# Optimization experiments

Measured on AMD Instinct MI355X. Metric: run time of the kernel, lower is better.

## Reference

```python
import jax, jax.numpy as jnp
import numpy as np

N_NODES = 50000
N_EDGES = 800000
IN_DIM = 128
HID = 128
N_GRAPHS = 64


def setup_inputs() -> dict:
    key = jax.random.key(0)
    ks = jax.random.split(key, 12)
    edge_index = jax.random.randint(ks[0], (2, N_EDGES), 0, N_NODES, dtype=jnp.int64)
    edge_weight = jax.random.uniform(ks[1], (N_EDGES,), dtype=jnp.float32)
    input_feature = jax.random.normal(ks[2], (N_NODES, IN_DIM), dtype=jnp.float32)
    graph_indicator = jnp.sort(jax.random.randint(ks[3], (N_NODES,), 0, N_GRAPHS, dtype=jnp.int64))
    s = 0.05
    W1 = jax.random.normal(ks[4], (IN_DIM, HID), dtype=jnp.float32) * s
    b1 = jnp.zeros((HID,), jnp.float32)
    W2 = jax.random.normal(ks[5], (HID, HID), dtype=jnp.float32) * s
    b2 = jnp.zeros((HID,), jnp.float32)
    W3 = jax.random.normal(ks[6], (HID, HID), dtype=jnp.float32) * s
    b3 = jnp.zeros((HID,), jnp.float32)
    wa = jax.random.normal(ks[7], (3 * HID, 1), dtype=jnp.float32) * s
    ba = jnp.zeros((1,), jnp.float32)
    Wf = jax.random.normal(ks[8], (3 * HID * 2, IN_DIM), dtype=jnp.float32) * s
    bf = jnp.zeros((IN_DIM,), jnp.float32)
    return dict(edge_index=edge_index, edge_weight=edge_weight,
                input_feature=input_feature, graph_indicator=graph_indicator,
                W1=W1, b1=b1, W2=W2, b2=b2, W3=W3, b3=b3,
                wa=wa, ba=ba, Wf=Wf, bf=bf)


def reference(edge_index, edge_weight, input_feature, graph_indicator,
              W1, b1, W2, b2, W3, b3, wa, ba, Wf, bf):
    src, dst = edge_index[0], edge_index[1]

    def gcn(x, W, b):
        # GraphConvolution: adj @ (x @ W) + b, adj given as weighted edge list
        support = x @ W  # [N, d_out]
        msg = edge_weight[:, None] * support[src]  # [E, d_out] gather
        return jax.ops.segment_sum(msg, dst, num_segments=N_NODES) + b

    g1 = jax.nn.relu(gcn(input_feature, W1, b1))
    g2 = jax.nn.relu(gcn(g1, W2, b2))
    g3 = jax.nn.relu(gcn(g2, W3, b3))
    h = jnp.concatenate([g1, g2, g3], axis=1)  # [N, 3*HID]

    # SelfAttentionPooling: attention score via a 1-dim GraphConvolution, tanh gate
    score = jnp.tanh(gcn(h, wa, ba))  # [N, 1]
    pool = h * score

    # segment avg / max pooling per graph
    seg_sum = jax.ops.segment_sum(pool, graph_indicator, num_segments=N_GRAPHS)
    counts = jax.ops.segment_sum(jnp.ones((N_NODES, 1), pool.dtype), graph_indicator,
                                 num_segments=N_GRAPHS)
    avg = seg_sum / jnp.maximum(counts, 1.0)
    mx = jax.ops.segment_max(pool, graph_indicator, num_segments=N_GRAPHS)
    pooled = jnp.concatenate([avg, mx], axis=1)  # [G, 6*HID]

    return jax.nn.relu(pooled @ Wf + bf)  # [G, IN_DIM]
```

## Files before the change

kernel.cpp:

```cpp
#include <hip/hip_runtime.h>
#include <math.h>

#define HID 128
#define POOL_SEG 16
#define WT_STRIDE 136
#define ELL_D 48
#define SC_CHUNK 2048
#define FXS 16384.0f
#define FXI (1.0f/16384.0f)

typedef __attribute__((ext_vector_type(8))) short short8;
typedef __attribute__((ext_vector_type(4))) float float4v;

__device__ inline short f2bf(float f) {
  unsigned u = __builtin_bit_cast(unsigned, f);
  unsigned r = (u + 0x7fff + ((u >> 16) & 1)) >> 16;
  return (short)r;
}
__device__ inline unsigned pack2bf(float lo, float hi) {
  return (unsigned)(unsigned short)f2bf(lo) | ((unsigned)(unsigned short)f2bf(hi) << 16);
}
__device__ inline float bflo(unsigned u) { return __builtin_bit_cast(float, u << 16); }
__device__ inline float bfhi(unsigned u) { return __builtin_bit_cast(float, u & 0xffff0000u); }
__device__ inline float bf2f(unsigned short s) { return __builtin_bit_cast(float, (unsigned)s << 16); }
__device__ inline unsigned short f2h(float f) {
  _Float16 h = (_Float16)f;
  return __builtin_bit_cast(unsigned short, h);
}
__device__ inline float h2f(unsigned short hb) {
  return (float)__builtin_bit_cast(_Float16, hb);
}

__global__ __launch_bounds__(256) void prologue(
    const void* __restrict__ ei_raw, const float* __restrict__ ew,
    int2* __restrict__ packed,
    const float* __restrict__ W1, const float* __restrict__ W2, const float* __restrict__ W3,
    short* __restrict__ T1, short* __restrict__ T2, short* __restrict__ T3,
    const void* __restrict__ gi_raw, int* __restrict__ gstart,
    int E, int N, int G, int EB) {
  int b = blockIdx.x, t = threadIdx.x;
  if (b < EB) {
    int e = b * 256 + t;
    if (e < E) {
      const int* pw = (const int*)ei_raw;
      int nz = 0;
#pragma unroll
      for (int i = 1; i < 64; i += 2) nz |= pw[i];
      int s, d;
      if (nz == 0) {
        const long long* p = (const long long*)ei_raw;
        s = (int)p[e]; d = (int)p[E + e];
      } else {
        const int* p = (const int*)ei_raw;
        s = p[e]; d = p[E + e];
      }
      packed[e] = make_int2((d << 16) | s, __builtin_bit_cast(int, ew[e]));
    }
  } else if (b < EB + 192) {
    int i = (b - EB) * 256 + t;
    int which = i >> 14, idx = i & 16383;
    int k = idx >> 7, nn = idx & 127;
    const float* W = (which == 0) ? W1 : ((which == 1) ? W2 : W3);
    short* T = (which == 0) ? T1 : ((which == 1) ? T2 : T3);
    T[nn * WT_STRIDE + k] = f2bf(W[idx]);
  } else {
    int g = t;
    if (g > G) return;
    if (g == G) { gstart[g] = N; return; }
    bool is64 = (((const int*)gi_raw)[N - 1] == 0);
    const long long* g64 = (const long long*)gi_raw;
    const int* g32 = (const int*)gi_raw;
    int lo = 0, hi = N;
    while (lo < hi) {
      int mid = (lo + hi) >> 1;
      long long v = is64 ? g64[mid] : (long long)g32[mid];
      if (v < (long long)g) lo = mid + 1; else hi = mid;
    }
    gstart[g] = lo;
  }
}

__global__ void scatter_ell(const int2* __restrict__ packed, int* __restrict__ cursor,
                            unsigned* __restrict__ ell, int E, int N) {
  int group = blockIdx.x & 7;
  int chunk = blockIdx.x >> 3;
  int rng = (N + 7) >> 3;
  int lo = group * rng;
  int hi = lo + rng; if (hi > N) hi = N;
  int base = chunk * SC_CHUNK;
  for (int i = 0; i < SC_CHUNK; i += 256) {
    int e = base + i + threadIdx.x;
    if (e < E) {
      int2 rec = packed[e];
      int d = ((unsigned)rec.x) >> 16;
      if (d >= lo && d < hi) {
        unsigned s = (unsigned)rec.x & 0xFFFFu;
        unsigned short wh = f2h(__builtin_bit_cast(float, rec.y));
        int pos = atomicAdd(&cursor[d], 1);
        if (pos < ELL_D)
          ell[(size_t)d * ELL_D + pos] = (s << 16) | (unsigned)wh;
      }
    }
  }
}

__global__ __launch_bounds__(256) void gemm_mfma(const float* __restrict__ Af,
                                                 const unsigned short* __restrict__ Abf,
                                                 const short* __restrict__ Wt,
                                                 unsigned short* __restrict__ C,
                                                 int n, int a_is_bf16) {
  __shared__ short Wlds[128 * WT_STRIDE];
  int t = threadIdx.x;
  {
    const ulonglong2* gsrc = (const ulonglong2*)Wt;
    ulonglong2* ldst = (ulonglong2*)Wlds;
    for (int i = t; i < (128 * WT_STRIDE) / 8; i += 256) ldst[i] = gsrc[i];
  }
  __syncthreads();

  int wave = t >> 6, lane = t & 63;
  int quad = lane >> 4, l15 = lane & 15;
  int m0 = blockIdx.x * 64 + wave * 16;
  size_t SL = (size_t)n * 32;

  int m = m0 + l15; if (m >= n) m = n - 1;
  short8 afrag[4];
  if (a_is_bf16) {
#pragma unroll
    for (int c = 0; c < 4; c++)
      afrag[c] = *(const short8*)(Abf + c * SL + (size_t)m * 32 + quad * 8);
  } else {
    const float* Arow = Af + (size_t)m * 128;
#pragma unroll
    for (int c = 0; c < 4; c++) {
      int k0 = c * 32 + quad * 8;
      float4 x = *(const float4*)(Arow + k0);
      float4 y = *(const float4*)(Arow + k0 + 4);
      short8 a;
      a[0] = f2bf(x.x); a[1] = f2bf(x.y); a[2] = f2bf(x.z); a[3] = f2bf(x.w);
      a[4] = f2bf(y.x); a[5] = f2bf(y.y); a[6] = f2bf(y.z); a[7] = f2bf(y.w);
      afrag[c] = a;
    }
  }

  float4v acc[8];
#pragma unroll
  for (int tt = 0; tt < 8; tt++) acc[tt] = (float4v){0.f, 0.f, 0.f, 0.f};

#pragma unroll
  for (int c = 0; c < 4; c++) {
    int kb = c * 32 + quad * 8;
#pragma unroll
    for (int tt = 0; tt < 8; tt++) {
      const short8* bp = (const short8*)&Wlds[(tt * 16 + l15) * WT_STRIDE + kb];
      acc[tt] = __builtin_amdgcn_mfma_f32_16x16x32_bf16(afrag[c], *bp, acc[tt], 0, 0, 0);
    }
  }

  int rbase = m0 + quad * 4;
#pragma unroll
  for (int tt = 0; tt < 8; tt++) {
    int within = (tt & 1) * 16 + l15;
    size_t sb = (size_t)(tt >> 1) * SL;
#pragma unroll
    for (int r = 0; r < 4; r++) {
      int row = rbase + r;
      if (row < n) C[sb + (size_t)row * 32 + within] = (unsigned short)f2bf(acc[tt][r]);
    }
  }
}

#define ACC8(wv, vv)                                                          \
  acc[0] += rintf(wv * bflo(vv.x)); acc[1] += rintf(wv * bfhi(vv.x));        \
  acc[2] += rintf(wv * bflo(vv.y)); acc[3] += rintf(wv * bfhi(vv.y));        \
  acc[4] += rintf(wv * bflo(vv.z)); acc[5] += rintf(wv * bfhi(vv.z));        \
  acc[6] += rintf(wv * bflo(vv.w)); acc[7] += rintf(wv * bfhi(vv.w));

__global__ __launch_bounds__(256) void aggregate_sl(
    const unsigned short* __restrict__ support, const int* __restrict__ deg_arr,
    const unsigned* __restrict__ ell, const float* __restrict__ bias,
    unsigned short* __restrict__ out,
    const unsigned short* __restrict__ g1p, const unsigned short* __restrict__ g2p,
    const float* __restrict__ wa, int* __restrict__ s_pre_fx,
    int n, int halfN, int do_score) {
  int group = blockIdx.x & 7;
  int slice = group >> 1, half = group & 1;
  int chunk = blockIdx.x >> 3;
  int t = threadIdx.x;
  int local = chunk * 64 + (t >> 2);
  int q = t & 3;
  if (local >= halfN) return;
  int node = half * halfN + local;
  if (node >= n) return;

  int deg = deg_arr[node]; if (deg > ELL_D) deg = ELL_D;
  const unsigned* row = ell + (size_t)node * ELL_D;
  const uint4* sb = (const uint4*)support + (size_t)slice * n * 4 + q;

  float acc[8];
#pragma unroll
  for (int j = 0; j < 8; j++) acc[j] = 0.f;

  int i = 0;
  for (; i + 7 < deg; i += 8) {
    uint4 ra = *(const uint4*)(row + i);
    uint4 rb = *(const uint4*)(row + i + 4);
    uint4 v0 = sb[(size_t)(ra.x >> 16) * 4];
    uint4 v1 = sb[(size_t)(ra.y >> 16) * 4];
    uint4 v2 = sb[(size_t)(ra.z >> 16) * 4];
    uint4 v3 = sb[(size_t)(ra.w >> 16) * 4];
    uint4 v4 = sb[(size_t)(rb.x >> 16) * 4];
    uint4 v5 = sb[(size_t)(rb.y >> 16) * 4];
    uint4 v6 = sb[(size_t)(rb.z >> 16) * 4];
    uint4 v7 = sb[(size_t)(rb.w >> 16) * 4];
    float w0 = h2f((unsigned short)(ra.x & 0xFFFF)) * FXS;
    float w1 = h2f((unsigned short)(ra.y & 0xFFFF)) * FXS;
    float w2 = h2f((unsigned short)(ra.z & 0xFFFF)) * FXS;
    float w3 = h2f((unsigned short)(ra.w & 0xFFFF)) * FXS;
    float w4 = h2f((unsigned short)(rb.x & 0xFFFF)) * FXS;
    float w5 = h2f((unsigned short)(rb.y & 0xFFFF)) * FXS;
    float w6 = h2f((unsigned short)(rb.z & 0xFFFF)) * FXS;
    float w7 = h2f((unsigned short)(rb.w & 0xFFFF)) * FXS;
    ACC8(w0, v0) ACC8(w1, v1) ACC8(w2, v2) ACC8(w3, v3)
    ACC8(w4, v4) ACC8(w5, v5) ACC8(w6, v6) ACC8(w7, v7)
  }
  for (; i + 3 < deg; i += 4) {
    uint4 ra = *(const uint4*)(row + i);
    uint4 v0 = sb[(size_t)(ra.x >> 16) * 4];
    uint4 v1 = sb[(size_t)(ra.y >> 16) * 4];
    uint4 v2 = sb[(size_t)(ra.z >> 16) * 4];
    uint4 v3 = sb[(size_t)(ra.w >> 16) * 4];
    float w0 = h2f((unsigned short)(ra.x & 0xFFFF)) * FXS;
    float w1 = h2f((unsigned short)(ra.y & 0xFFFF)) * FXS;
    float w2 = h2f((unsigned short)(ra.z & 0xFFFF)) * FXS;
    float w3 = h2f((unsigned short)(ra.w & 0xFFFF)) * FXS;
    ACC8(w0, v0) ACC8(w1, v1) ACC8(w2, v2) ACC8(w3, v3)
  }
  for (; i < deg; i++) {
    unsigned r0 = row[i];
    float w0 = h2f((unsigned short)(r0 & 0xFFFF)) * FXS;
    uint4 v0 = sb[(size_t)(r0 >> 16) * 4];
    ACC8(w0, v0)
  }

  float f[8];
#pragma unroll
  for (int j = 0; j < 8; j++) f[j] = acc[j] * FXI;

  float4 b0 = ((const float4*)bias)[slice * 8 + q * 2];
  float4 b1 = ((const float4*)bias)[slice * 8 + q * 2 + 1];
  f[0] = fmaxf(f[0] + b0.x, 0.f); f[1] = fmaxf(f[1] + b0.y, 0.f);
  f[2] = fmaxf(f[2] + b0.z, 0.f); f[3] = fmaxf(f[3] + b0.w, 0.f);
  f[4] = fmaxf(f[4] + b1.x, 0.f); f[5] = fmaxf(f[5] + b1.y, 0.f);
  f[6] = fmaxf(f[6] + b1.z, 0.f); f[7] = fmaxf(f[7] + b1.w, 0.f);

  uint4 o;
  o.x = pack2bf(f[0], f[1]); o.y = pack2bf(f[2], f[3]);
  o.z = pack2bf(f[4], f[5]); o.w = pack2bf(f[6], f[7]);
  ((uint4*)out)[(size_t)slice * n * 4 + (size_t)node * 4 + q] = o;

  if (do_score) {
    uint4 u1 = ((const uint4*)g1p)[(size_t)slice * n * 4 + (size_t)node * 4 + q];
    uint4 u2 = ((const uint4*)g2p)[(size_t)slice * n * 4 + (size_t)node * 4 + q];
    const float* wa1 = wa + slice * 32 + q * 8;
    const float* wa2 = wa1 + 128;
    const float* wa3 = wa1 + 256;
    float sc = bflo(u1.x) * wa1[0] + bfhi(u1.x) * wa1[1]
             + bflo(u1.y) * wa1[2] + bfhi(u1.y) * wa1[3]
             + bflo(u1.z) * wa1[4] + bfhi(u1.z) * wa1[5]
             + bflo(u1.w) * wa1[6] + bfhi(u1.w) * wa1[7]
             + bflo(u2.x) * wa2[0] + bfhi(u2.x) * wa2[1]
             + bflo(u2.y) * wa2[2] + bfhi(u2.y) * wa2[3]
             + bflo(u2.z) * wa2[4] + bfhi(u2.z) * wa2[5]
             + bflo(u2.w) * wa2[6] + bfhi(u2.w) * wa2[7];
#pragma unroll
    for (int j = 0; j < 8; j++) sc += f[j] * wa3[j];
    sc += __shfl_xor(sc, 1, 64);
    sc += __shfl_xor(sc, 2, 64);
    if (q == 0) atomicAdd(&s_pre_fx[node], __float2int_rn(sc * FXS));
  }
}

__global__ __launch_bounds__(384) void pool_partial(const unsigned short* __restrict__ g1,
                                                    const unsigned short* __restrict__ g2,
                                                    const unsigned short* __restrict__ g3,
                                                    const int* __restrict__ s_pre_fx,
                                                    const int* __restrict__ deg_arr,
                                                    const unsigned* __restrict__ ell,
                                                    const float* __restrict__ ba,
                                                    const int* __restrict__ gstart,
                                                    float* __restrict__ part, int n) {
  int g = blockIdx.x / POOL_SEG, seg = blockIdx.x % POOL_SEG;
  int t = threadIdx.x;
  int sg = t >> 7, dd = t & 127;
  const unsigned short* gp = (sg == 0) ? g1 : ((sg == 1) ? g2 : g3);
  const unsigned short* col = gp + (size_t)(dd >> 5) * ((size_t)n * 32) + (dd & 31);
  int s = gstart[g], e = gstart[g + 1];
  int len = e - s;
  int chunk = (len + POOL_SEG - 1) / POOL_SEG;
  int ns = s + seg * chunk;
  int ne = ns + chunk; if (ne > e) ne = e;
  float ba0 = ba[0];
  __shared__ float sc_lds[256];
  float sum = 0.f, mx = -3.402823466e38f;
  for (int tb = ns; tb < ne; tb += 256) {
    int te = tb + 256; if (te > ne) te = ne;
    __syncthreads();
    if (t < te - tb) {
      int node = tb + t;
      int deg = deg_arr[node]; if (deg > ELL_D) deg = ELL_D;
      const unsigned* row = ell + (size_t)node * ELL_D;
      float acc = 0.f;
      for (int i = 0; i < deg; i++) {
        unsigned r = row[i];
        acc += rintf(h2f((unsigned short)(r & 0xFFFF)) * (float)s_pre_fx[r >> 16]);
      }
      sc_lds[t] = tanhf(acc * FXI + ba0);
    }
    __syncthreads();
    for (int node = tb; node < te; node++) {
      float v = bf2f(col[(size_t)node * 32]) * sc_lds[node - tb];
      sum += v;
      mx = fmaxf(mx, v);
    }
  }
  size_t base = (size_t)blockIdx.x * 768;
  part[base + t] = sum;
  part[base + 384 + t] = mx;
}

__global__ __launch_bounds__(512) void tail(const float* __restrict__ part,
                                            const int* __restrict__ gstart,
                                            const float* __restrict__ Wf,
                                            const float* __restrict__ bfb,
                                            float* __restrict__ out) {
  __shared__ float pooled[768];
  __shared__ float red[512];
  int g = blockIdx.x, t = threadIdx.x;
  float cnt = (float)(gstart[g + 1] - gstart[g]);
  float inv = 1.0f / fmaxf(cnt, 1.0f);
  if (t < 384) {
    int d = t;
    float sum = 0.f, mx = -3.402823466e38f;
    for (int seg = 0; seg < POOL_SEG; seg++) {
      size_t base = ((size_t)g * POOL_SEG + seg) * 768;
      sum += part[base + d];
      mx = fmaxf(mx, part[base + 384 + d]);
    }
    pooled[d] = sum * inv;
    pooled[384 + d] = mx;
  }
  __syncthreads();
  int kc = t >> 7, c = t & 127;
  float acc = (kc == 0) ? bfb[c] : 0.f;
  int k0 = kc * 192;
#pragma unroll 8
  for (int k = k0; k < k0 + 192; k++) acc += pooled[k] * Wf[(size_t)k * 128 + c];
  red[t] = acc;
  __syncthreads();
  if (t < 128)
    out[(size_t)g * 128 + t] =
        fmaxf(red[t] + red[t + 128] + red[t + 256] + red[t + 384], 0.f);
}

extern "C" void kernel_launch(void* const* d_in, const int* in_sizes, int n_in,
                              void* d_out, int out_size, void* d_ws, size_t ws_size,
                              hipStream_t stream) {
  const void* ei_raw = d_in[0];
  const float* ew    = (const float*)d_in[1];
  const float* X     = (const float*)d_in[2];
  const void* gi_raw = d_in[3];
  const float* W1 = (const float*)d_in[4];  const float* b1 = (const float*)d_in[5];
  const float* W2 = (const float*)d_in[6];  const float* b2 = (const float*)d_in[7];
  const float* W3 = (const float*)d_in[8];  const float* b3 = (const float*)d_in[9];
  const float* wa = (const float*)d_in[10]; const float* ba = (const float*)d_in[11];
  const float* Wf = (const float*)d_in[12]; const float* bf = (const float*)d_in[13];
  float* out = (float*)d_out;

  const int E = in_sizes[1];
  const int N = in_sizes[2] / 128;
  const int G = out_size / 128;

  char* ws = (char*)d_ws;
  size_t off = 0;
  auto take = [&](size_t bytes) {
    char* p = ws + off;
    off = (off + bytes + 255) & ~(size_t)255;
    return p;
  };
  int* zb = (int*)take((size_t)N * 8);
  int* cursor   = zb;
  int* s_pre_fx = zb + N;
  int2* packed  = (int2*)take((size_t)E * 8);
  unsigned* ell = (unsigned*)take((size_t)N * ELL_D * 4);
  short*    wt1 = (short*)take((size_t)128 * WT_STRIDE * 2);
  short*    wt2 = (short*)take((size_t)128 * WT_STRIDE * 2);
  short*    wt3 = (short*)take((size_t)128 * WT_STRIDE * 2);
  unsigned short* support = (unsigned short*)take((size_t)N * 128 * 2);
  unsigned short* g1      = (unsigned short*)take((size_t)N * 128 * 2);
  unsigned short* g2      = (unsigned short*)take((size_t)N * 128 * 2);
  unsigned short* g3      = (unsigned short*)take((size_t)N * 128 * 2);
  int*   gstart  = (int*)take((size_t)(G + 1) * 4);
  float* part    = (float*)take((size_t)G * POOL_SEG * 768 * 4);
  if (off > ws_size) return;

  hipMemsetAsync(zb, 0, (size_t)N * 8, stream);

  const int EB = (E + 255) / 256;
  prologue<<<EB + 192 + 1, 256, 0, stream>>>(ei_raw, ew, packed,
                                             W1, W2, W3, wt1, wt2, wt3,
                                             gi_raw, gstart, E, N, G, EB);
  {
    int chunks = (E + SC_CHUNK - 1) / SC_CHUNK;
    scatter_ell<<<8 * chunks, 256, 0, stream>>>(packed, cursor, ell, E, N);
  }

  const int GB = (N + 63) / 64;
  const int halfN = (N + 1) / 2;
  const int AGB = 8 * ((halfN + 63) / 64);
  gemm_mfma<<<GB, 256, 0, stream>>>(X, (const unsigned short*)nullptr, wt1, support, N, 0);
  aggregate_sl<<<AGB, 256, 0, stream>>>(support, cursor, ell, b1, g1,
                                        nullptr, nullptr, nullptr, nullptr, N, halfN, 0);
  gemm_mfma<<<GB, 256, 0, stream>>>((const float*)nullptr, g1, wt2, support, N, 1);
  aggregate_sl<<<AGB, 256, 0, stream>>>(support, cursor, ell, b2, g2,
                                        nullptr, nullptr, nullptr, nullptr, N, halfN, 0);
  gemm_mfma<<<GB, 256, 0, stream>>>((const float*)nullptr, g2, wt3, support, N, 1);
  aggregate_sl<<<AGB, 256, 0, stream>>>(support, cursor, ell, b3, g3,
                                        g1, g2, wa, s_pre_fx, N, halfN, 1);

  pool_partial<<<G * POOL_SEG, 384, 0, stream>>>(g1, g2, g3, s_pre_fx, cursor, ell,
                                                 ba, gstart, part, N);
  tail<<<G, 512, 0, stream>>>(part, gstart, Wf, bf, out);
}
```

Measured before the change: 318.6 us.

## Fuse memset into prologue, scatter into first GEMM, and tail into pool

```diff
diff --git a/kernel.cpp b/kernel.cpp
--- a/kernel.cpp
+++ b/kernel.cpp
@@ -33,15 +33,17 @@
 
 __global__ __launch_bounds__(256) void prologue(
     const void* __restrict__ ei_raw, const float* __restrict__ ew,
-    int2* __restrict__ packed,
+    int2* __restrict__ packed, int* __restrict__ cursor, int* __restrict__ s_pre_fx,
+    int* __restrict__ pool_done,
     const float* __restrict__ W1, const float* __restrict__ W2, const float* __restrict__ W3,
     short* __restrict__ T1, short* __restrict__ T2, short* __restrict__ T3,
     const void* __restrict__ gi_raw, int* __restrict__ gstart,
     int E, int N, int G, int EB) {
   int b = blockIdx.x, t = threadIdx.x;
   if (b < EB) {
-    int e = b * 256 + t;
-    if (e < E) {
+    int gid = b * 256 + t;
+    if (gid < N) { cursor[gid] = 0; s_pre_fx[gid] = 0; }
+    if (gid < E) {
       const int* pw = (const int*)ei_raw;
       int nz = 0;
 #pragma unroll
@@ -49,12 +51,12 @@
       int s, d;
       if (nz == 0) {
         const long long* p = (const long long*)ei_raw;
-        s = (int)p[e]; d = (int)p[E + e];
+        s = (int)p[gid]; d = (int)p[E + gid];
       } else {
         const int* p = (const int*)ei_raw;
-        s = p[e]; d = p[E + e];
+        s = p[gid]; d = p[E + gid];
       }
-      packed[e] = make_int2((d << 16) | s, __builtin_bit_cast(int, ew[e]));
+      packed[gid] = make_int2((d << 16) | s, __builtin_bit_cast(int, ew[gid]));
     }
   } else if (b < EB + 192) {
     int i = (b - EB) * 256 + t;
@@ -65,6 +67,7 @@
     T[nn * WT_STRIDE + k] = f2bf(W[idx]);
   } else {
     int g = t;
+    if (g < G) pool_done[g] = 0;
     if (g > G) return;
     if (g == G) { gstart[g] = N; return; }
     bool is64 = (((const int*)gi_raw)[N - 1] == 0);
@@ -80,35 +83,38 @@
   }
 }
 
-__global__ void scatter_ell(const int2* __restrict__ packed, int* __restrict__ cursor,
-                            unsigned* __restrict__ ell, int E, int N) {
-  int group = blockIdx.x & 7;
-  int chunk = blockIdx.x >> 3;
-  int rng = (N + 7) >> 3;
-  int lo = group * rng;
-  int hi = lo + rng; if (hi > N) hi = N;
-  int base = chunk * SC_CHUNK;
-  for (int i = 0; i < SC_CHUNK; i += 256) {
-    int e = base + i + threadIdx.x;
-    if (e < E) {
-      int2 rec = packed[e];
-      int d = ((unsigned)rec.x) >> 16;
-      if (d >= lo && d < hi) {
-        unsigned s = (unsigned)rec.x & 0xFFFFu;
-        unsigned short wh = f2h(__builtin_bit_cast(float, rec.y));
-        int pos = atomicAdd(&cursor[d], 1);
-        if (pos < ELL_D)
-          ell[(size_t)d * ELL_D + pos] = (s << 16) | (unsigned)wh;
-      }
-    }
-  }
-}
-
 __global__ __launch_bounds__(256) void gemm_mfma(const float* __restrict__ Af,
                                                  const unsigned short* __restrict__ Abf,
                                                  const short* __restrict__ Wt,
                                                  unsigned short* __restrict__ C,
-                                                 int n, int a_is_bf16) {
+                                                 int n, int a_is_bf16, int gemm_nb,
+                                                 const int2* __restrict__ packed,
+                                                 int* __restrict__ cursor,
+                                                 unsigned* __restrict__ ell, int E) {
+  if (blockIdx.x >= gemm_nb) {
+    int sb = blockIdx.x - gemm_nb;
+    int group = sb & 7;
+    int chunk = sb >> 3;
+    int rng = (n + 7) >> 3;
+    int lo = group * rng;
+    int hi = lo + rng; if (hi > n) hi = n;
+    int base = chunk * SC_CHUNK;
+    for (int i = 0; i < SC_CHUNK; i += 256) {
+      int e = base + i + threadIdx.x;
+      if (e < E) {
+        int2 rec = packed[e];
+        int d = ((unsigned)rec.x) >> 16;
+        if (d >= lo && d < hi) {
+          unsigned s = (unsigned)rec.x & 0xFFFFu;
+          unsigned short wh = f2h(__builtin_bit_cast(float, rec.y));
+          int pos = atomicAdd(&cursor[d], 1);
+          if (pos < ELL_D)
+            ell[(size_t)d * ELL_D + pos] = (s << 16) | (unsigned)wh;
+        }
+      }
+    }
+    return;
+  }
   __shared__ short Wlds[128 * WT_STRIDE];
   int t = threadIdx.x;
   {
@@ -281,15 +287,19 @@
   }
 }
 
-__global__ __launch_bounds__(384) void pool_partial(const unsigned short* __restrict__ g1,
-                                                    const unsigned short* __restrict__ g2,
-                                                    const unsigned short* __restrict__ g3,
-                                                    const int* __restrict__ s_pre_fx,
-                                                    const int* __restrict__ deg_arr,
-                                                    const unsigned* __restrict__ ell,
-                                                    const float* __restrict__ ba,
-                                                    const int* __restrict__ gstart,
-                                                    float* __restrict__ part, int n) {
+__global__ __launch_bounds__(384) void pool_tail(const unsigned short* __restrict__ g1,
+                                                 const unsigned short* __restrict__ g2,
+                                                 const unsigned short* __restrict__ g3,
+                                                 const int* __restrict__ s_pre_fx,
+                                                 const int* __restrict__ deg_arr,
+                                                 const unsigned* __restrict__ ell,
+                                                 const float* __restrict__ ba,
+                                                 const int* __restrict__ gstart,
+                                                 float* __restrict__ part,
+                                                 int* __restrict__ pool_done,
+                                                 const float* __restrict__ Wf,
+                                                 const float* __restrict__ bfb,
+                                                 float* __restrict__ out, int n) {
   int g = blockIdx.x / POOL_SEG, seg = blockIdx.x % POOL_SEG;
   int t = threadIdx.x;
   int sg = t >> 7, dd = t & 127;
@@ -327,40 +337,40 @@
   size_t base = (size_t)blockIdx.x * 768;
   part[base + t] = sum;
   part[base + 384 + t] = mx;
-}
-
-__global__ __launch_bounds__(512) void tail(const float* __restrict__ part,
-                                            const int* __restrict__ gstart,
-                                            const float* __restrict__ Wf,
-                                            const float* __restrict__ bfb,
-                                            float* __restrict__ out) {
+
+  __threadfence();
+  __shared__ int is_last;
+  __syncthreads();
+  if (t == 0) is_last = (atomicAdd(&pool_done[g], 1) == POOL_SEG - 1) ? 1 : 0;
+  __syncthreads();
+  if (!is_last) return;
+  __threadfence();
+
   __shared__ float pooled[768];
-  __shared__ float red[512];
-  int g = blockIdx.x, t = threadIdx.x;
-  float cnt = (float)(gstart[g + 1] - gstart[g]);
+  __shared__ float red[384];
+  float cnt = (float)len;
   float inv = 1.0f / fmaxf(cnt, 1.0f);
-  if (t < 384) {
+  {
     int d = t;
-    float sum = 0.f, mx = -3.402823466e38f;
-    for (int seg = 0; seg < POOL_SEG; seg++) {
-      size_t base = ((size_t)g * POOL_SEG + seg) * 768;
-      sum += part[base + d];
-      mx = fmaxf(mx, part[base + 384 + d]);
-    }
-    pooled[d] = sum * inv;
-    pooled[384 + d] = mx;
+    float ssum = 0.f, smx = -3.402823466e38f;
+    for (int sg2 = 0; sg2 < POOL_SEG; sg2++) {
+      size_t b2 = ((size_t)g * POOL_SEG + sg2) * 768;
+      ssum += part[b2 + d];
+      smx = fmaxf(smx, part[b2 + 384 + d]);
+    }
+    pooled[d] = ssum * inv;
+    pooled[384 + d] = smx;
   }
   __syncthreads();
   int kc = t >> 7, c = t & 127;
   float acc = (kc == 0) ? bfb[c] : 0.f;
-  int k0 = kc * 192;
+  int k0 = kc * 256;
 #pragma unroll 8
-  for (int k = k0; k < k0 + 192; k++) acc += pooled[k] * Wf[(size_t)k * 128 + c];
+  for (int k = k0; k < k0 + 256; k++) acc += pooled[k] * Wf[(size_t)k * 128 + c];
   red[t] = acc;
   __syncthreads();
   if (t < 128)
-    out[(size_t)g * 128 + t] =
-        fmaxf(red[t] + red[t + 128] + red[t + 256] + red[t + 384], 0.f);
+    out[(size_t)g * 128 + t] = fmaxf(red[t] + red[t + 128] + red[t + 256], 0.f);
 }
 
 extern "C" void kernel_launch(void* const* d_in, const int* in_sizes, int n_in,
@@ -388,9 +398,8 @@
     off = (off + bytes + 255) & ~(size_t)255;
     return p;
   };
-  int* zb = (int*)take((size_t)N * 8);
-  int* cursor   = zb;
-  int* s_pre_fx = zb + N;
+  int* cursor   = (int*)take((size_t)N * 4);
+  int* s_pre_fx = (int*)take((size_t)N * 4);
   int2* packed  = (int2*)take((size_t)E * 8);
   unsigned* ell = (unsigned*)take((size_t)N * ELL_D * 4);
   short*    wt1 = (short*)take((size_t)128 * WT_STRIDE * 2);
@@ -400,35 +409,33 @@
   unsigned short* g1      = (unsigned short*)take((size_t)N * 128 * 2);
   unsigned short* g2      = (unsigned short*)take((size_t)N * 128 * 2);
   unsigned short* g3      = (unsigned short*)take((size_t)N * 128 * 2);
-  int*   gstart  = (int*)take((size_t)(G + 1) * 4);
-  float* part    = (float*)take((size_t)G * POOL_SEG * 768 * 4);
+  int*   gstart    = (int*)take((size_t)(G + 1) * 4);
+  int*   pool_done = (int*)take((size_t)G * 4);
+  float* part      = (float*)take((size_t)G * POOL_SEG * 768 * 4);
   if (off > ws_size) return;
 
-  hipMemsetAsync(zb, 0, (size_t)N * 8, stream);
-
   const int EB = (E + 255) / 256;
-  prologue<<<EB + 192 + 1, 256, 0, stream>>>(ei_raw, ew, packed,
-                                             W1, W2, W3, wt1, wt2, wt3,
+  prologue<<<EB + 192 + 1, 256, 0, stream>>>(ei_raw, ew, packed, cursor, s_pre_fx,
+                                             pool_done, W1, W2, W3, wt1, wt2, wt3,
                                              gi_raw, gstart, E, N, G, EB);
-  {
-    int chunks = (E + SC_CHUNK - 1) / SC_CHUNK;
-    scatter_ell<<<8 * chunks, 256, 0, stream>>>(packed, cursor, ell, E, N);
-  }
 
   const int GB = (N + 63) / 64;
   const int halfN = (N + 1) / 2;
   const int AGB = 8 * ((halfN + 63) / 64);
-  gemm_mfma<<<GB, 256, 0, stream>>>(X, (const unsigned short*)nullptr, wt1, support, N, 0);
+  const int chunks = (E + SC_CHUNK - 1) / SC_CHUNK;
+  gemm_mfma<<<GB + 8 * chunks, 256, 0, stream>>>(X, (const unsigned short*)nullptr, wt1,
+                                                 support, N, 0, GB, packed, cursor, ell, E);
   aggregate_sl<<<AGB, 256, 0, stream>>>(support, cursor, ell, b1, g1,
                                         nullptr, nullptr, nullptr, nullptr, N, halfN, 0);
-  gemm_mfma<<<GB, 256, 0, stream>>>((const float*)nullptr, g1, wt2, support, N, 1);
+  gemm_mfma<<<GB, 256, 0, stream>>>((const float*)nullptr, g1, wt2, support, N, 1, GB,
+                                    nullptr, nullptr, nullptr, 0);
   aggregate_sl<<<AGB, 256, 0, stream>>>(support, cursor, ell, b2, g2,
                                         nullptr, nullptr, nullptr, nullptr, N, halfN, 0);
-  gemm_mfma<<<GB, 256, 0, stream>>>((const float*)nullptr, g2, wt3, support, N, 1);
+  gemm_mfma<<<GB, 256, 0, stream>>>((const float*)nullptr, g2, wt3, support, N, 1, GB,
+                                    nullptr, nullptr, nullptr, 0);
   aggregate_sl<<<AGB, 256, 0, stream>>>(support, cursor, ell, b3, g3,
                                         g1, g2, wa, s_pre_fx, N, halfN, 1);
 
-  pool_partial<<<G * POOL_SEG, 384, 0, stream>>>(g1, g2, g3, s_pre_fx, cursor, ell,
-                                                 ba, gstart, part, N);
-  tail<<<G, 512, 0, stream>>>(part, gstart, Wf, bf, out);
-}
+  pool_tail<<<G * POOL_SEG, 384, 0, stream>>>(g1, g2, g3, s_pre_fx, cursor, ell,
+                                              ba, gstart, part, pool_done, Wf, bf, out, N);
+}
```

Measured after the change: 444.8 us. 1.4x slower.

## Fuse ELL scatter into first GEMM launch and zero buffers in prologue

Applied to the files above, without the earlier changes.

```diff
diff --git a/kernel.cpp b/kernel.cpp
--- a/kernel.cpp
+++ b/kernel.cpp
@@ -33,15 +33,16 @@
 
 __global__ __launch_bounds__(256) void prologue(
     const void* __restrict__ ei_raw, const float* __restrict__ ew,
-    int2* __restrict__ packed,
+    int2* __restrict__ packed, int* __restrict__ cursor, int* __restrict__ s_pre_fx,
     const float* __restrict__ W1, const float* __restrict__ W2, const float* __restrict__ W3,
     short* __restrict__ T1, short* __restrict__ T2, short* __restrict__ T3,
     const void* __restrict__ gi_raw, int* __restrict__ gstart,
     int E, int N, int G, int EB) {
   int b = blockIdx.x, t = threadIdx.x;
   if (b < EB) {
-    int e = b * 256 + t;
-    if (e < E) {
+    int gid = b * 256 + t;
+    if (gid < N) { cursor[gid] = 0; s_pre_fx[gid] = 0; }
+    if (gid < E) {
       const int* pw = (const int*)ei_raw;
       int nz = 0;
 #pragma unroll
@@ -49,12 +50,12 @@
       int s, d;
       if (nz == 0) {
         const long long* p = (const long long*)ei_raw;
-        s = (int)p[e]; d = (int)p[E + e];
+        s = (int)p[gid]; d = (int)p[E + gid];
       } else {
         const int* p = (const int*)ei_raw;
-        s = p[e]; d = p[E + e];
+        s = p[gid]; d = p[E + gid];
       }
-      packed[e] = make_int2((d << 16) | s, __builtin_bit_cast(int, ew[e]));
+      packed[gid] = make_int2((d << 16) | s, __builtin_bit_cast(int, ew[gid]));
     }
   } else if (b < EB + 192) {
     int i = (b - EB) * 256 + t;
@@ -80,35 +81,38 @@
   }
 }
 
-__global__ void scatter_ell(const int2* __restrict__ packed, int* __restrict__ cursor,
-                            unsigned* __restrict__ ell, int E, int N) {
-  int group = blockIdx.x & 7;
-  int chunk = blockIdx.x >> 3;
-  int rng = (N + 7) >> 3;
-  int lo = group * rng;
-  int hi = lo + rng; if (hi > N) hi = N;
-  int base = chunk * SC_CHUNK;
-  for (int i = 0; i < SC_CHUNK; i += 256) {
-    int e = base + i + threadIdx.x;
-    if (e < E) {
-      int2 rec = packed[e];
-      int d = ((unsigned)rec.x) >> 16;
-      if (d >= lo && d < hi) {
-        unsigned s = (unsigned)rec.x & 0xFFFFu;
-        unsigned short wh = f2h(__builtin_bit_cast(float, rec.y));
-        int pos = atomicAdd(&cursor[d], 1);
-        if (pos < ELL_D)
-          ell[(size_t)d * ELL_D + pos] = (s << 16) | (unsigned)wh;
-      }
-    }
-  }
-}
-
 __global__ __launch_bounds__(256) void gemm_mfma(const float* __restrict__ Af,
                                                  const unsigned short* __restrict__ Abf,
                                                  const short* __restrict__ Wt,
                                                  unsigned short* __restrict__ C,
-                                                 int n, int a_is_bf16) {
+                                                 int n, int a_is_bf16, int gemm_nb,
+                                                 const int2* __restrict__ packed,
+                                                 int* __restrict__ cursor,
+                                                 unsigned* __restrict__ ell, int E) {
+  if (blockIdx.x >= gemm_nb) {
+    int sb = blockIdx.x - gemm_nb;
+    int group = sb & 7;
+    int chunk = sb >> 3;
+    int rng = (n + 7) >> 3;
+    int lo = group * rng;
+    int hi = lo + rng; if (hi > n) hi = n;
+    int base = chunk * SC_CHUNK;
+    for (int i = 0; i < SC_CHUNK; i += 256) {
+      int e = base + i + threadIdx.x;
+      if (e < E) {
+        int2 rec = packed[e];
+        int d = ((unsigned)rec.x) >> 16;
+        if (d >= lo && d < hi) {
+          unsigned s = (unsigned)rec.x & 0xFFFFu;
+          unsigned short wh = f2h(__builtin_bit_cast(float, rec.y));
+          int pos = atomicAdd(&cursor[d], 1);
+          if (pos < ELL_D)
+            ell[(size_t)d * ELL_D + pos] = (s << 16) | (unsigned)wh;
+        }
+      }
+    }
+    return;
+  }
   __shared__ short Wlds[128 * WT_STRIDE];
   int t = threadIdx.x;
   {
@@ -388,9 +392,8 @@
     off = (off + bytes + 255) & ~(size_t)255;
     return p;
   };
-  int* zb = (int*)take((size_t)N * 8);
-  int* cursor   = zb;
-  int* s_pre_fx = zb + N;
+  int* cursor   = (int*)take((size_t)N * 4);
+  int* s_pre_fx = (int*)take((size_t)N * 4);
   int2* packed  = (int2*)take((size_t)E * 8);
   unsigned* ell = (unsigned*)take((size_t)N * ELL_D * 4);
   short*    wt1 = (short*)take((size_t)128 * WT_STRIDE * 2);
@@ -404,27 +407,25 @@
   float* part    = (float*)take((size_t)G * POOL_SEG * 768 * 4);
   if (off > ws_size) return;
 
-  hipMemsetAsync(zb, 0, (size_t)N * 8, stream);
-
   const int EB = (E + 255) / 256;
-  prologue<<<EB + 192 + 1, 256, 0, stream>>>(ei_raw, ew, packed,
+  prologue<<<EB + 192 + 1, 256, 0, stream>>>(ei_raw, ew, packed, cursor, s_pre_fx,
                                              W1, W2, W3, wt1, wt2, wt3,
                                              gi_raw, gstart, E, N, G, EB);
-  {
-    int chunks = (E + SC_CHUNK - 1) / SC_CHUNK;
-    scatter_ell<<<8 * chunks, 256, 0, stream>>>(packed, cursor, ell, E, N);
-  }
 
   const int GB = (N + 63) / 64;
   const int halfN = (N + 1) / 2;
   const int AGB = 8 * ((halfN + 63) / 64);
-  gemm_mfma<<<GB, 256, 0, stream>>>(X, (const unsigned short*)nullptr, wt1, support, N, 0);
+  const int chunks = (E + SC_CHUNK - 1) / SC_CHUNK;
+  gemm_mfma<<<GB + 8 * chunks, 256, 0, stream>>>(X, (const unsigned short*)nullptr, wt1,
+                                                 support, N, 0, GB, packed, cursor, ell, E);
   aggregate_sl<<<AGB, 256, 0, stream>>>(support, cursor, ell, b1, g1,
                                         nullptr, nullptr, nullptr, nullptr, N, halfN, 0);
-  gemm_mfma<<<GB, 256, 0, stream>>>((const float*)nullptr, g1, wt2, support, N, 1);
+  gemm_mfma<<<GB, 256, 0, stream>>>((const float*)nullptr, g1, wt2, support, N, 1, GB,
+                                    nullptr, nullptr, nullptr, 0);
   aggregate_sl<<<AGB, 256, 0, stream>>>(support, cursor, ell, b2, g2,
                                         nullptr, nullptr, nullptr, nullptr, N, halfN, 0);
-  gemm_mfma<<<GB, 256, 0, stream>>>((const float*)nullptr, g2, wt3, support, N, 1);
+  gemm_mfma<<<GB, 256, 0, stream>>>((const float*)nullptr, g2, wt3, support, N, 1, GB,
+                                    nullptr, nullptr, nullptr, 0);
   aggregate_sl<<<AGB, 256, 0, stream>>>(support, cursor, ell, b3, g3,
                                         g1, g2, wa, s_pre_fx, N, halfN, 1);
 
```

New measurement: 310.4 us. -2.6%, faster.

## Fuse prologue, ELL scatter and first GEMM into one launch; unroll aggregation by 16

Applied to the files above, without the earlier changes.

```diff
diff --git a/kernel.cpp b/kernel.cpp
--- a/kernel.cpp
+++ b/kernel.cpp
@@ -31,90 +31,77 @@
   return (float)__builtin_bit_cast(_Float16, hb);
 }
 
-__global__ __launch_bounds__(256) void prologue(
+__global__ __launch_bounds__(256) void mega1(
+    const float* __restrict__ Af, const short* __restrict__ WtUnused,
+    unsigned short* __restrict__ C, int n, int gemm_nb,
     const void* __restrict__ ei_raw, const float* __restrict__ ew,
-    int2* __restrict__ packed,
+    int* __restrict__ cursor, unsigned* __restrict__ ell, int E, int scb,
     const float* __restrict__ W1, const float* __restrict__ W2, const float* __restrict__ W3,
-    short* __restrict__ T1, short* __restrict__ T2, short* __restrict__ T3,
-    const void* __restrict__ gi_raw, int* __restrict__ gstart,
-    int E, int N, int G, int EB) {
-  int b = blockIdx.x, t = threadIdx.x;
-  if (b < EB) {
-    int e = b * 256 + t;
-    if (e < E) {
+    short* __restrict__ T2, short* __restrict__ T3,
+    const void* __restrict__ gi_raw, int* __restrict__ gstart, int G) {
+  int t = threadIdx.x;
+  if (blockIdx.x >= gemm_nb) {
+    int b2 = blockIdx.x - gemm_nb;
+    if (b2 < scb) {
+      int group = b2 & 7;
+      int chunk = b2 >> 3;
+      int rng = (n + 7) >> 3;
+      int lo = group * rng;
+      int hi = lo + rng; if (hi > n) hi = n;
       const int* pw = (const int*)ei_raw;
       int nz = 0;
 #pragma unroll
       for (int i = 1; i < 64; i += 2) nz |= pw[i];
-      int s, d;
-      if (nz == 0) {
-        const long long* p = (const long long*)ei_raw;
-        s = (int)p[e]; d = (int)p[E + e];
-      } else {
-        const int* p = (const int*)ei_raw;
-        s = p[e]; d = p[E + e];
+      bool is64 = (nz == 0);
+      const long long* p64 = (const long long*)ei_raw;
+      const int* p32 = (const int*)ei_raw;
+      int base = chunk * SC_CHUNK;
+      for (int i = 0; i < SC_CHUNK; i += 256) {
+        int e = base + i + t;
+        if (e < E) {
+          int s, d;
+          if (is64) { s = (int)p64[e]; d = (int)p64[E + e]; }
+          else      { s = p32[e];      d = p32[E + e]; }
+          if (d >= lo && d < hi) {
+            unsigned short wh = f2h(ew[e]);
+            int pos = atomicAdd(&cursor[d], 1);
+            if (pos < ELL_D)
+              ell[(size_t)d * ELL_D + pos] = ((unsigned)s << 16) | (unsigned)wh;
+          }
+        }
       }
-      packed[e] = make_int2((d << 16) | s, __builtin_bit_cast(int, ew[e]));
-    }
-  } else if (b < EB + 192) {
-    int i = (b - EB) * 256 + t;
-    int which = i >> 14, idx = i & 16383;
-    int k = idx >> 7, nn = idx & 127;
-    const float* W = (which == 0) ? W1 : ((which == 1) ? W2 : W3);
-    short* T = (which == 0) ? T1 : ((which == 1) ? T2 : T3);
-    T[nn * WT_STRIDE + k] = f2bf(W[idx]);
-  } else {
+      return;
+    }
+    b2 -= scb;
+    if (b2 < 128) {
+      int i = b2 * 256 + t;
+      int which = i >> 14, idx = i & 16383;
+      int k = idx >> 7, nn = idx & 127;
+      const float* W = (which == 0) ? W2 : W3;
+      short* T = (which == 0) ? T2 : T3;
+      T[nn * WT_STRIDE + k] = f2bf(W[idx]);
+      return;
+    }
     int g = t;
     if (g > G) return;
-    if (g == G) { gstart[g] = N; return; }
-    bool is64 = (((const int*)gi_raw)[N - 1] == 0);
+    if (g == G) { gstart[g] = n; return; }
+    bool gis64 = (((const int*)gi_raw)[n - 1] == 0);
     const long long* g64 = (const long long*)gi_raw;
     const int* g32 = (const int*)gi_raw;
-    int lo = 0, hi = N;
+    int lo = 0, hi = n;
     while (lo < hi) {
       int mid = (lo + hi) >> 1;
-      long long v = is64 ? g64[mid] : (long long)g32[mid];
+      long long v = gis64 ? g64[mid] : (long long)g32[mid];
       if (v < (long long)g) lo = mid + 1; else hi = mid;
     }
     gstart[g] = lo;
-  }
-}
-
-__global__ void scatter_ell(const int2* __restrict__ packed, int* __restrict__ cursor,
-                            unsigned* __restrict__ ell, int E, int N) {
-  int group = blockIdx.x & 7;
-  int chunk = blockIdx.x >> 3;
-  int rng = (N + 7) >> 3;
-  int lo = group * rng;
-  int hi = lo + rng; if (hi > N) hi = N;
-  int base = chunk * SC_CHUNK;
-  for (int i = 0; i < SC_CHUNK; i += 256) {
-    int e = base + i + threadIdx.x;
-    if (e < E) {
-      int2 rec = packed[e];
-      int d = ((unsigned)rec.x) >> 16;
-      if (d >= lo && d < hi) {
-        unsigned s = (unsigned)rec.x & 0xFFFFu;
-        unsigned short wh = f2h(__builtin_bit_cast(float, rec.y));
-        int pos = atomicAdd(&cursor[d], 1);
-        if (pos < ELL_D)
-          ell[(size_t)d * ELL_D + pos] = (s << 16) | (unsigned)wh;
-      }
-    }
-  }
-}
-
-__global__ __launch_bounds__(256) void gemm_mfma(const float* __restrict__ Af,
-                                                 const unsigned short* __restrict__ Abf,
-                                                 const short* __restrict__ Wt,
-                                                 unsigned short* __restrict__ C,
-                                                 int n, int a_is_bf16) {
+    return;
+  }
+
   __shared__ short Wlds[128 * WT_STRIDE];
-  int t = threadIdx.x;
-  {
-    const ulonglong2* gsrc = (const ulonglong2*)Wt;
-    ulonglong2* ldst = (ulonglong2*)Wlds;
-    for (int i = t; i < (128 * WT_STRIDE) / 8; i += 256) ldst[i] = gsrc[i];
+  for (int idx = t; idx < 16384; idx += 256) {
+    int k = idx >> 7, nn = idx & 127;
+    Wlds[nn * WT_STRIDE + k] = f2bf(W1[idx]);
   }
   __syncthreads();
 
@@ -125,11 +112,7 @@
 
   int m = m0 + l15; if (m >= n) m = n - 1;
   short8 afrag[4];
-  if (a_is_bf16) {
-#pragma unroll
-    for (int c = 0; c < 4; c++)
-      afrag[c] = *(const short8*)(Abf + c * SL + (size_t)m * 32 + quad * 8);
-  } else {
+  {
     const float* Arow = Af + (size_t)m * 128;
 #pragma unroll
     for (int c = 0; c < 4; c++) {
@@ -170,13 +153,63 @@
   }
 }
 
+__global__ __launch_bounds__(256) void gemm_mfma(const unsigned short* __restrict__ Abf,
+                                                 const short* __restrict__ Wt,
+                                                 unsigned short* __restrict__ C, int n) {
+  __shared__ short Wlds[128 * WT_STRIDE];
+  int t = threadIdx.x;
+  {
+    const ulonglong2* gsrc = (const ulonglong2*)Wt;
+    ulonglong2* ldst = (ulonglong2*)Wlds;
+    for (int i = t; i < (128 * WT_STRIDE) / 8; i += 256) ldst[i] = gsrc[i];
+  }
+  __syncthreads();
+
+  int wave = t >> 6, lane = t & 63;
+  int quad = lane >> 4, l15 = lane & 15;
+  int m0 = blockIdx.x * 64 + wave * 16;
+  size_t SL = (size_t)n * 32;
+
+  int m = m0 + l15; if (m >= n) m = n - 1;
+  short8 afrag[4];
+#pragma unroll
+  for (int c = 0; c < 4; c++)
+    afrag[c] = *(const short8*)(Abf + c * SL + (size_t)m * 32 + quad * 8);
+
+  float4v acc[8];
+#pragma unroll
+  for (int tt = 0; tt < 8; tt++) acc[tt] = (float4v){0.f, 0.f, 0.f, 0.f};
+
+#pragma unroll
+  for (int c = 0; c < 4; c++) {
+    int kb = c * 32 + quad * 8;
+#pragma unroll
+    for (int tt = 0; tt < 8; tt++) {
+      const short8* bp = (const short8*)&Wlds[(tt * 16 + l15) * WT_STRIDE + kb];
+      acc[tt] = __builtin_amdgcn_mfma_f32_16x16x32_bf16(afrag[c], *bp, acc[tt], 0, 0, 0);
+    }
+  }
+
+  int rbase = m0 + quad * 4;
+#pragma unroll
+  for (int tt = 0; tt < 8; tt++) {
+    int within = (tt & 1) * 16 + l15;
+    size_t sb = (size_t)(tt >> 1) * SL;
+#pragma unroll
+    for (int r = 0; r < 4; r++) {
+      int row = rbase + r;
+      if (row < n) C[sb + (size_t)row * 32 + within] = (unsigned short)f2bf(acc[tt][r]);
+    }
+  }
+}
+
 #define ACC8(wv, vv)                                                          \
   acc[0] += rintf(wv * bflo(vv.x)); acc[1] += rintf(wv * bfhi(vv.x));        \
   acc[2] += rintf(wv * bflo(vv.y)); acc[3] += rintf(wv * bfhi(vv.y));        \
   acc[4] += rintf(wv * bflo(vv.z)); acc[5] += rintf(wv * bfhi(vv.z));        \
   acc[6] += rintf(wv * bflo(vv.w)); acc[7] += rintf(wv * bfhi(vv.w));
 
-__global__ __launch_bounds__(256) void aggregate_sl(
+__global__ __launch_bounds__(256, 4) void aggregate_sl(
     const unsigned short* __restrict__ support, const int* __restrict__ deg_arr,
     const unsigned* __restrict__ ell, const float* __restrict__ bias,
     unsigned short* __restrict__ out,
@@ -202,6 +235,48 @@
   for (int j = 0; j < 8; j++) acc[j] = 0.f;
 
   int i = 0;
+  for (; i + 15 < deg; i += 16) {
+    uint4 ra = *(const uint4*)(row + i);
+    uint4 rb = *(const uint4*)(row + i + 4);
+    uint4 rc = *(const uint4*)(row + i + 8);
+    uint4 rd = *(const uint4*)(row + i + 12);
+    uint4 v0 = sb[(size_t)(ra.x >> 16) * 4];
+    uint4 v1 = sb[(size_t)(ra.y >> 16) * 4];
+    uint4 v2 = sb[(size_t)(ra.z >> 16) * 4];
+    uint4 v3 = sb[(size_t)(ra.w >> 16) * 4];
+    uint4 v4 = sb[(size_t)(rb.x >> 16) * 4];
+    uint4 v5 = sb[(size_t)(rb.y >> 16) * 4];
+    uint4 v6 = sb[(size_t)(rb.z >> 16) * 4];
+    uint4 v7 = sb[(size_t)(rb.w >> 16) * 4];
+    uint4 v8 = sb[(size_t)(rc.x >> 16) * 4];
+    uint4 v9 = sb[(size_t)(rc.y >> 16) * 4];
+    uint4 vA = sb[(size_t)(rc.z >> 16) * 4];
+    uint4 vB = sb[(size_t)(rc.w >> 16) * 4];
+    uint4 vC = sb[(size_t)(rd.x >> 16) * 4];
+    uint4 vD = sb[(size_t)(rd.y >> 16) * 4];
+    uint4 vE = sb[(size_t)(rd.z >> 16) * 4];
+    uint4 vF = sb[(size_t)(rd.w >> 16) * 4];
+    float w0 = h2f((unsigned short)(ra.x & 0xFFFF)) * FXS;
+    float w1 = h2f((unsigned short)(ra.y & 0xFFFF)) * FXS;
+    float w2 = h2f((unsigned short)(ra.z & 0xFFFF)) * FXS;
+    float w3 = h2f((unsigned short)(ra.w & 0xFFFF)) * FXS;
+    float w4 = h2f((unsigned short)(rb.x & 0xFFFF)) * FXS;
+    float w5 = h2f((unsigned short)(rb.y & 0xFFFF)) * FXS;
+    float w6 = h2f((unsigned short)(rb.z & 0xFFFF)) * FXS;
+    float w7 = h2f((unsigned short)(rb.w & 0xFFFF)) * FXS;
+    float w8 = h2f((unsigned short)(rc.x & 0xFFFF)) * FXS;
+    float w9 = h2f((unsigned short)(rc.y & 0xFFFF)) * FXS;
+    float wA = h2f((unsigned short)(rc.z & 0xFFFF)) * FXS;
+    float wB = h2f((unsigned short)(rc.w & 0xFFFF)) * FXS;
+    float wC = h2f((unsigned short)(rd.x & 0xFFFF)) * FXS;
+    float wD = h2f((unsigned short)(rd.y & 0xFFFF)) * FXS;
+    float wE = h2f((unsigned short)(rd.z & 0xFFFF)) * FXS;
+    float wF = h2f((unsigned short)(rd.w & 0xFFFF)) * FXS;
+    ACC8(w0, v0) ACC8(w1, v1) ACC8(w2, v2) ACC8(w3, v3)
+    ACC8(w4, v4) ACC8(w5, v5) ACC8(w6, v6) ACC8(w7, v7)
+    ACC8(w8, v8) ACC8(w9, v9) ACC8(wA, vA) ACC8(wB, vB)
+    ACC8(wC, vC) ACC8(wD, vD) ACC8(wE, vE) ACC8(wF, vF)
+  }
   for (; i + 7 < deg; i += 8) {
     uint4 ra = *(const uint4*)(row + i);
     uint4 rb = *(const uint4*)(row + i + 4);
@@ -391,9 +466,7 @@
   int* zb = (int*)take((size_t)N * 8);
   int* cursor   = zb;
   int* s_pre_fx = zb + N;
-  int2* packed  = (int2*)take((size_t)E * 8);
   unsigned* ell = (unsigned*)take((size_t)N * ELL_D * 4);
-  short*    wt1 = (short*)take((size_t)128 * WT_STRIDE * 2);
   short*    wt2 = (short*)take((size_t)128 * WT_STRIDE * 2);
   short*    wt3 = (short*)take((size_t)128 * WT_STRIDE * 2);
   unsigned short* support = (unsigned short*)take((size_t)N * 128 * 2);
@@ -406,25 +479,21 @@
 
   hipMemsetAsync(zb, 0, (size_t)N * 8, stream);
 
-  const int EB = (E + 255) / 256;
-  prologue<<<EB + 192 + 1, 256, 0, stream>>>(ei_raw, ew, packed,
-                                             W1, W2, W3, wt1, wt2, wt3,
-                                             gi_raw, gstart, E, N, G, EB);
-  {
-    int chunks = (E + SC_CHUNK - 1) / SC_CHUNK;
-    scatter_ell<<<8 * chunks, 256, 0, stream>>>(packed, cursor, ell, E, N);
-  }
-
   const int GB = (N + 63) / 64;
   const int halfN = (N + 1) / 2;
   const int AGB = 8 * ((halfN + 63) / 64);
-  gemm_mfma<<<GB, 256, 0, stream>>>(X, (const unsigned short*)nullptr, wt1, support, N, 0);
+  const int chunks = (E + SC_CHUNK - 1) / SC_CHUNK;
+  const int SCB = 8 * chunks;
+  mega1<<<GB + SCB + 128 + 1, 256, 0, stream>>>(X, nullptr, support, N, GB,
+                                                ei_raw, ew, cursor, ell, E, SCB,
+                                                W1, W2, W3, wt2, wt3,
+                                                gi_raw, gstart, G);
   aggregate_sl<<<AGB, 256, 0, stream>>>(support, cursor, ell, b1, g1,
                                         nullptr, nullptr, nullptr, nullptr, N, halfN, 0);
-  gemm_mfma<<<GB, 256, 0, stream>>>((const float*)nullptr, g1, wt2, support, N, 1);
+  gemm_mfma<<<GB, 256, 0, stream>>>(g1, wt2, support, N);
   aggregate_sl<<<AGB, 256, 0, stream>>>(support, cursor, ell, b2, g2,
                                         nullptr, nullptr, nullptr, nullptr, N, halfN, 0);
-  gemm_mfma<<<GB, 256, 0, stream>>>((const float*)nullptr, g2, wt3, support, N, 1);
+  gemm_mfma<<<GB, 256, 0, stream>>>(g2, wt3, support, N);
   aggregate_sl<<<AGB, 256, 0, stream>>>(support, cursor, ell, b3, g3,
                                         g1, g2, wa, s_pre_fx, N, halfN, 1);
 
```

New measurement: 313.1 us. Within noise of the previous version (-1.7%).
